# Optimization experiments

Measured on AMD Instinct MI355X. Metric: run time of the kernel, lower is better.

## Reference

```python
import jax, jax.numpy as jnp
import numpy as np

B, C, H, W = 8, 256, 64, 64
E, D, K = 4, 4, 2
CR = C // 16  # CBAM channel-attention reduction ratio 16

def _conv(x, w, pad):
    return jax.lax.conv_general_dilated(
        x, w, (1, 1), [(pad, pad), (pad, pad)],
        dimension_numbers=('NCHW', 'OIHW', 'NCHW'))

def _bn(x, s, b):  # eval-mode BatchNorm folded into per-channel affine
    return x * s[None, :, None, None] + b[None, :, None, None]

def _expert(p, x, dom_ids):
    # domain_transform: conv3x3-BN-GELU-conv3x3-BN
    h = jax.nn.gelu(_bn(_conv(x, p['dt_w1'], 1), p['dt_bn1s'], p['dt_bn1b']))
    d = _bn(_conv(h, p['dt_w2'], 1), p['dt_bn2s'], p['dt_bn2b'])
    # domain_gate: GAP -> conv1x1 C->1 -> sigmoid
    g1 = jax.nn.sigmoid(jnp.mean(d, (2, 3)) @ p['gate_w'] + p['gate_b'])  # [B]
    out = x + g1[:, None, None, None] * d
    # Res_CBAM_block (in==out channels, stride 1 -> identity shortcut)
    r = out
    h = jax.nn.relu(_bn(_conv(out, p['c1_w'], 1) + p['c1_b'][None, :, None, None], p['bn1s'], p['bn1b']))
    h = _bn(_conv(h, p['c2_w'], 1) + p['c2_b'][None, :, None, None], p['bn2s'], p['bn2b'])
    # channel attention (shared MLP over GAP and GMP)
    avg, mx = jnp.mean(h, (2, 3)), jnp.max(h, (2, 3))
    mlp = lambda v: jax.nn.relu(v @ p['ca_w1'].T) @ p['ca_w2'].T
    ca = jax.nn.sigmoid(mlp(avg) + mlp(mx))  # [B,C]
    h = h * ca[:, :, None, None]
    # spatial attention: 7x7 conv over [mean_c, max_c]
    sa_in = jnp.concatenate([jnp.mean(h, 1, keepdims=True), jnp.max(h, 1, keepdims=True)], axis=1)
    sa = jax.nn.sigmoid(_conv(sa_in, p['sa_w'], 3))
    h = jax.nn.relu(h * sa + r)
    # per-domain adapter bias (nn.Embedding lookup)
    return h + p['adp'][dom_ids][:, :, None, None]

def _forward(x, domain_ids, g_w1, g_b1, ln_s, ln_b, g_w2, g_b2, dom_emb,
             e_dt_w1, e_dt_bn1s, e_dt_bn1b, e_dt_w2, e_dt_bn2s, e_dt_bn2b,
             e_gate_w, e_gate_b, e_c1_w, e_c1_b, e_bn1s, e_bn1b,
             e_c2_w, e_c2_b, e_bn2s, e_bn2b, e_ca_w1, e_ca_w2, e_sa_w, e_adapter):
    ep = dict(dt_w1=e_dt_w1, dt_bn1s=e_dt_bn1s, dt_bn1b=e_dt_bn1b,
              dt_w2=e_dt_w2, dt_bn2s=e_dt_bn2s, dt_bn2b=e_dt_bn2b,
              gate_w=e_gate_w, gate_b=e_gate_b,
              c1_w=e_c1_w, c1_b=e_c1_b, bn1s=e_bn1s, bn1b=e_bn1b,
              c2_w=e_c2_w, c2_b=e_c2_b, bn2s=e_bn2s, bn2b=e_bn2b,
              ca_w1=e_ca_w1, ca_w2=e_ca_w2, sa_w=e_sa_w, adp=e_adapter)
    eouts = jax.vmap(_expert, in_axes=(0, None, None))(ep, x, domain_ids)  # [E,B,C,H,W]
    # gate input: [GAP(x) | GMP(x) | domain_embed(16)] -> Linear -> LN -> ReLU -> Linear -> softmax
    gi = jnp.concatenate([jnp.mean(x, (2, 3)), jnp.max(x, (2, 3)), dom_emb[domain_ids]], axis=1)
    hg = gi @ g_w1 + g_b1
    mu = jnp.mean(hg, -1, keepdims=True)
    var = jnp.var(hg, -1, keepdims=True)
    hg = jax.nn.relu((hg - mu) * jax.lax.rsqrt(var + 1e-5) * ln_s + ln_b)
    probs = jax.nn.softmax(hg @ g_w2 + g_b2, axis=-1)  # [B,E]
    vals, idx = jax.lax.top_k(probs, K)                # soft top-k routing
    wk = vals / jnp.sum(vals, -1, keepdims=True)       # renormalize top-k weights
    wfull = jnp.zeros_like(probs).at[jnp.arange(probs.shape[0])[:, None], idx].set(wk)
    return jnp.einsum('be,ebchw->bchw', wfull, eouts)

def setup_inputs():
    key = jax.random.key(0)
    ks = iter(jax.random.split(key, 48))
    rn = lambda shape, s=0.05: jax.random.normal(next(ks), shape, jnp.float32) * s
    p = {}
    p['x'] = jax.random.normal(next(ks), (B, C, H, W), jnp.float32)
    p['domain_ids'] = jax.random.randint(next(ks), (B,), 0, D)
    p['g_w1'] = rn((2 * C + 16, C)); p['g_b1'] = jnp.zeros((C,))
    p['ln_s'] = jnp.ones((C,)); p['ln_b'] = jnp.zeros((C,))
    p['g_w2'] = rn((C, E)); p['g_b2'] = jnp.zeros((E,))
    p['dom_emb'] = rn((D, 16), 0.5)
    p['e_dt_w1'] = rn((E, C, C, 3, 3)); p['e_dt_bn1s'] = jnp.ones((E, C)); p['e_dt_bn1b'] = jnp.zeros((E, C))
    p['e_dt_w2'] = rn((E, C, C, 3, 3)); p['e_dt_bn2s'] = jnp.ones((E, C)); p['e_dt_bn2b'] = jnp.zeros((E, C))
    p['e_gate_w'] = rn((E, C)); p['e_gate_b'] = jnp.zeros((E,))
    p['e_c1_w'] = rn((E, C, C, 3, 3)); p['e_c1_b'] = jnp.zeros((E, C))
    p['e_bn1s'] = jnp.ones((E, C)); p['e_bn1b'] = jnp.zeros((E, C))
    p['e_c2_w'] = rn((E, C, C, 3, 3)); p['e_c2_b'] = jnp.zeros((E, C))
    p['e_bn2s'] = jnp.ones((E, C)); p['e_bn2b'] = jnp.zeros((E, C))
    p['e_ca_w1'] = rn((E, CR, C)); p['e_ca_w2'] = rn((E, C, CR))
    p['e_sa_w'] = rn((E, 1, 2, 7, 7))
    p['e_adapter'] = rn((E, D, C), 0.1)
    return p

def reference(x, domain_ids, g_w1, g_b1, ln_s, ln_b, g_w2, g_b2, dom_emb,
              e_dt_w1, e_dt_bn1s, e_dt_bn1b, e_dt_w2, e_dt_bn2s, e_dt_bn2b,
              e_gate_w, e_gate_b, e_c1_w, e_c1_b, e_bn1s, e_bn1b,
              e_c2_w, e_c2_b, e_bn2s, e_bn2b, e_ca_w1, e_ca_w2, e_sa_w, e_adapter):
    return _forward(x, domain_ids, g_w1, g_b1, ln_s, ln_b, g_w2, g_b2, dom_emb,
                    e_dt_w1, e_dt_bn1s, e_dt_bn1b, e_dt_w2, e_dt_bn2s, e_dt_bn2b,
                    e_gate_w, e_gate_b, e_c1_w, e_c1_b, e_bn1s, e_bn1b,
                    e_c2_w, e_c2_b, e_bn2s, e_bn2b, e_ca_w1, e_ca_w2, e_sa_w, e_adapter)
```

## Files before the change

kernel.cpp:

```cpp
#include <hip/hip_runtime.h>
#include <math.h>

typedef __bf16 bf16x8 __attribute__((ext_vector_type(8)));
typedef float  f32x4  __attribute__((ext_vector_type(4)));

#define NB 8
#define NC 256
#define NHW 4096
#define NCHW_ 1048576
#define NSLOT 16

__device__ __forceinline__ float sigmoidf_(float x){ return 1.f/(1.f+expf(-x)); }
__device__ __forceinline__ float gelu_tanh(float x){
  float x3 = x*x*x;
  return 0.5f*x*(1.f+tanhf(0.7978845608028654f*(x + 0.044715f*x3)));
}

__device__ __forceinline__ void gload16(const void* g, void* l){
  __builtin_amdgcn_global_load_lds((const __attribute__((address_space(1))) void*)g,
                                   (__attribute__((address_space(3))) void*)l,
                                   16, 0, 0);
}

__global__ void k_prep_sb(const float* dt_bn1s, const float* dt_bn1b,
                          const float* dt_bn2s, const float* dt_bn2b,
                          const float* c1_b, const float* bn1s, const float* bn1b,
                          const float* c2_b, const float* bn2s, const float* bn2b,
                          float* effS, float* effB){
  int ec = blockIdx.x; int e = ec>>2, cv = ec&3; int c = threadIdx.x;
  int i = e*NC + c;
  float s, b;
  if (cv==0){ s = dt_bn1s[i]; b = dt_bn1b[i]; }
  else if (cv==1){ s = dt_bn2s[i]; b = dt_bn2b[i]; }
  else if (cv==2){ s = bn1s[i]; b = c1_b[i]*bn1s[i] + bn1b[i]; }
  else { s = bn2s[i]; b = c2_b[i]*bn2s[i] + bn2b[i]; }
  effS[ec*NC+c]=s; effB[ec*NC+c]=b;
}

__global__ void k_prep_w(const float* w0, const float* w1, const float* w2, const float* w3,
                         __bf16* wr){
  __shared__ float tl[9][257];
  int o = blockIdx.x; int ec = blockIdx.y; int e = ec>>2, cv = ec&3;
  int t = threadIdx.x;
  const float* src = (cv==0)?w0 : (cv==1)?w1 : (cv==2)?w2 : w3;
  const float* sp = src + ((size_t)((e*NC + o)*NC + t))*9;
  #pragma unroll
  for (int k=0;k<9;k++) tl[k][t] = sp[k];
  __syncthreads();
  __bf16* dst = wr + (size_t)ec*589824 + (size_t)o*256;
  #pragma unroll
  for (int k=0;k<9;k++) dst[(size_t)k*65536 + t] = (__bf16)tl[k][t];
}

__global__ void k_prep_x(const float* x, __bf16* xh){
  __shared__ float tl[32][33];
  int p0 = blockIdx.x*32, c0 = blockIdx.y*32, b = blockIdx.z;
  int tx = threadIdx.x&31, ty = threadIdx.x>>5;
  #pragma unroll
  for (int k=0;k<4;k++){
    int c = c0 + ty + k*8;
    tl[ty+k*8][tx] = x[(size_t)(b*NC+c)*NHW + p0 + tx];
  }
  __syncthreads();
  #pragma unroll
  for (int k=0;k<4;k++){
    int p = p0 + ty + k*8;
    xh[(size_t)b*NCHW_ + (size_t)p*NC + c0 + tx] = (__bf16)tl[tx][ty+k*8];
  }
}

__global__ void k_gate1(const float* x, float* gavg, float* gmax){
  __shared__ float rs[256], rm[256];
  int bc = blockIdx.x; int t = threadIdx.x;
  const float* base = x + (size_t)bc*NHW;
  float s=0.f, m=-1e30f;
  #pragma unroll
  for (int k=0;k<16;k++){ float v = base[t + k*256]; s+=v; m=fmaxf(m,v); }
  rs[t]=s; rm[t]=m; __syncthreads();
  for (int st=128; st; st>>=1){ if (t<st){ rs[t]+=rs[t+st]; rm[t]=fmaxf(rm[t],rm[t+st]); } __syncthreads(); }
  if (t==0){ gavg[bc]=rs[0]/4096.f; gmax[bc]=rm[0]; }
}

__global__ void k_gate2(const float* gavg, const float* gmax, const int* dom,
                        const float* dom_emb, const float* w1, const float* b1,
                        const float* lns, const float* lnb,
                        const float* w2, const float* b2,
                        int* slot_e, float* slot_w){
  __shared__ float gi[8][528];
  __shared__ float hg[8][256];
  __shared__ float stat[16];
  __shared__ float logit[8][4];
  int t = threadIdx.x;
  for (int idx=t; idx<8*528; idx+=256){
    int b = idx/528, k = idx - b*528;
    float v;
    if (k<256) v = gavg[b*256+k];
    else if (k<512) v = gmax[b*256+k-256];
    else v = dom_emb[dom[b]*16 + (k-512)];
    gi[b][k]=v;
  }
  __syncthreads();
  for (int b=0;b<8;b++){
    float acc = b1[t];
    for (int k=0;k<528;k++) acc += gi[b][k]*w1[k*256+t];
    hg[b][t]=acc;
  }
  __syncthreads();
  if (t<8){
    float mu=0.f; for(int c=0;c<256;c++) mu += hg[t][c]; mu/=256.f;
    float vr=0.f; for(int c=0;c<256;c++){ float d=hg[t][c]-mu; vr+=d*d; } vr/=256.f;
    stat[t]=mu; stat[8+t]=vr;
  }
  __syncthreads();
  for (int b=0;b<8;b++){
    float v = (hg[b][t]-stat[b])*rsqrtf(stat[8+b]+1e-5f)*lns[t]+lnb[t];
    hg[b][t] = fmaxf(v, 0.f);
  }
  __syncthreads();
  if (t<32){
    int b = t>>2, e = t&3;
    float acc = b2[e];
    for (int c=0;c<256;c++) acc += hg[b][c]*w2[c*4+e];
    logit[b][e]=acc;
  }
  __syncthreads();
  if (t==0){
    for (int b=0;b<8;b++){
      float mx = logit[b][0];
      for (int e=1;e<4;e++) mx = fmaxf(mx, logit[b][e]);
      float p[4], s=0.f;
      for (int e=0;e<4;e++){ p[e]=expf(logit[b][e]-mx); s+=p[e]; }
      for (int e=0;e<4;e++) p[e]/=s;
      int i0=0; for (int e=1;e<4;e++) if (p[e]>p[i0]) i0=e;
      int i1=-1; for (int e=0;e<4;e++){ if (e==i0) continue; if (i1<0 || p[e]>p[i1]) i1=e; }
      float den = p[i0]+p[i1];
      slot_e[2*b]   = i0; slot_w[2*b]   = p[i0]/den;
      slot_e[2*b+1] = i1; slot_w[2*b+1] = p[i1]/den;
    }
  }
}

template<int ACT>
__global__ __launch_bounds__(256,2) void k_conv(
    const __bf16* __restrict__ in0, int per_b,
    const __bf16* __restrict__ wr,  int conv_idx,
    const float* __restrict__ effS, const float* __restrict__ effB,
    const int* __restrict__ slot_e,
    const __bf16* __restrict__ zslab,
    __bf16* __restrict__ out)
{
  __shared__ __bf16 smem[17408];
  __bf16* lA = smem;
  __bf16* lB = smem + 8192;

  const int tid   = threadIdx.x;
  const int slot  = blockIdx.y;
  const int e     = slot_e[slot];
  const int tileM = blockIdx.x & 1;
  const int tileN = blockIdx.x >> 1;
  const int cout_base = tileM*128;
  const int pos_base  = tileN*128;
  const int lane   = tid & 63;
  const int wv     = tid >> 6;
  const int lane15 = lane & 15, quad = lane >> 4;
  const int m_off  = (wv&1)*64, n_off = (wv>>1)*64;

  const __bf16* in = in0 + (size_t)(per_b ? (slot>>1) : slot) * NCHW_;
  const __bf16* wb = wr + (size_t)(e*4 + conv_idx) * 589824;

  int ldsOff[4];
  int aOff[4];
  int bBase[4];
  int rr0[4], cl0[4];
  #pragma unroll
  for (int j=0;j<4;j++){
    int f = (wv*4+j)*64 + lane;
    int row = f>>3, ph = f&7;
    int lc = ph ^ (row&7);
    ldsOff[j] = f*8;
    aOff[j]   = (cout_base + row)*256 + lc*8;
    int gp = pos_base + row;
    rr0[j] = gp>>6; cl0[j] = gp&63;
    bBase[j] = lc*8;
  }

  f32x4 zero = {0.f,0.f,0.f,0.f};
  f32x4 acc[4][4];
  #pragma unroll
  for (int i=0;i<4;i++)
    #pragma unroll
    for (int j=0;j<4;j++) acc[i][j] = zero;

  const int ph_read = lane15 & 7;

  for (int kk=0; kk<36; ++kk){
    const int k9 = kk>>2, c0e = (kk&3)*64;
    const int k3 = k9/3;
    const int dy = k3 - 1, dx = k9 - k3*3 - 1;
    __syncthreads();
    {
      const __bf16* ws = wb + (size_t)k9*65536 + c0e;
      #pragma unroll
      for (int j=0;j<4;j++)
        gload16(ws + aOff[j], lA + ldsOff[j]);
    }
    {
      const int doff = dy*16384 + dx*256 + c0e;
      #pragma unroll
      for (int j=0;j<4;j++){
        int rr = rr0[j] + dy, cl = cl0[j] + dx;
        const __bf16* src = ((unsigned)rr < 64u && (unsigned)cl < 64u)
            ? in + (size_t)(rr0[j]*16384 + cl0[j]*256 + doff + bBase[j])
            : zslab;
        gload16(src, lB + ldsOff[j]);
      }
    }
    __syncthreads();
    #pragma unroll
    for (int s=0;s<2;s++){
      bf16x8 af[4], bfr[4];
      const int ph = (s*4 + quad) ^ ph_read;
      #pragma unroll
      for (int i=0;i<4;i++) af[i]  = *(const bf16x8*)(lA + (m_off + i*16 + lane15)*64 + ph*8);
      #pragma unroll
      for (int j=0;j<4;j++) bfr[j] = *(const bf16x8*)(lB + (n_off + j*16 + lane15)*64 + ph*8);
      #pragma unroll
      for (int i=0;i<4;i++)
        #pragma unroll
        for (int j=0;j<4;j++)
          acc[i][j] = __builtin_amdgcn_mfma_f32_16x16x32_bf16(af[i], bfr[j], acc[i][j], 0,0,0);
    }
  }
  __syncthreads();

  const float* sS = effS + (e*4+conv_idx)*256 + cout_base;
  const float* sB = effB + (e*4+conv_idx)*256 + cout_base;
  float sc[16], bi[16];
  #pragma unroll
  for (int i=0;i<4;i++)
    #pragma unroll
    for (int r=0;r<4;r++){
      int m = m_off + i*16 + quad*4 + r;
      sc[i*4+r] = sS[m]; bi[i*4+r] = sB[m];
    }
  __bf16* lO = smem;
  #pragma unroll
  for (int i=0;i<4;i++){
    #pragma unroll
    for (int j=0;j<4;j++){
      int n = n_off + j*16 + lane15;
      #pragma unroll
      for (int r=0;r<4;r++){
        int m = m_off + i*16 + quad*4 + r;
        float v = acc[i][j][r]*sc[i*4+r] + bi[i*4+r];
        if (ACT==1) v = gelu_tanh(v);
        if (ACT==2) v = fmaxf(v, 0.f);
        lO[n*136 + m] = (__bf16)v;
      }
    }
  }
  __syncthreads();
  __bf16* ob = out + (size_t)slot*NCHW_;
  #pragma unroll
  for (int h=0; h<8; ++h){
    int chunk = tid + h*256;
    int prow = chunk>>4, part = chunk&15;
    *(uint4*)(ob + (size_t)(pos_base+prow)*256 + cout_base + part*8) =
      *(const uint4*)(lO + prow*136 + part*8);
  }
}

__global__ void k_g1red(const __bf16* d, const float* gate_w, const int* slot_e, float* p_sum){
  __shared__ float red[256];
  int chunk = blockIdx.x, slot = blockIdx.y, t = threadIdx.x;
  int e = slot_e[slot];
  const __bf16* base = d + (size_t)slot*NCHW_ + (size_t)chunk*512*256;
  float s = 0.f;
  for (int p=0;p<512;p++) s += (float)base[(size_t)p*256 + t];
  s *= gate_w[e*256+t];
  red[t]=s; __syncthreads();
  for (int st=128; st; st>>=1){ if (t<st) red[t]+=red[t+st]; __syncthreads(); }
  if (t==0) p_sum[slot*8+chunk]=red[0];
}

__global__ void k_pw_r(const __bf16* xh, const __bf16* d, const float* p_sum,
                       const float* gate_b, const int* slot_e, __bf16* r){
  int slot = blockIdx.y;
  int idx = blockIdx.x*256 + threadIdx.x;
  float tot = 0.f;
  #pragma unroll
  for (int k=0;k<8;k++) tot += p_sum[slot*8+k];
  int e = slot_e[slot];
  float g1 = sigmoidf_(tot/4096.f + gate_b[e]);
  size_t o = (size_t)slot*NCHW_ + idx;
  r[o] = (__bf16)((float)xh[(size_t)(slot>>1)*NCHW_ + idx] + g1*(float)d[o]);
}

__global__ void k_ca1(const __bf16* h3, float* ps, float* pm){
  int chunk = blockIdx.x, slot = blockIdx.y, t = threadIdx.x;
  const __bf16* base = h3 + (size_t)slot*NCHW_ + (size_t)chunk*512*256;
  float s=0.f, m=-1e30f;
  for (int p=0;p<512;p++){ float v = (float)base[(size_t)p*256+t]; s+=v; m=fmaxf(m,v); }
  ps[(slot*8+chunk)*256+t]=s; pm[(slot*8+chunk)*256+t]=m;
}

__global__ void k_ca2(const float* ps, const float* pm, const float* w1, const float* w2,
                      const int* slot_e, float* ca){
  __shared__ float avg[256], mxs[256], hr[32];
  int slot = blockIdx.x, t = threadIdx.x;
  int e = slot_e[slot];
  float s=0.f, m=-1e30f;
  #pragma unroll
  for (int k=0;k<8;k++){ s += ps[(slot*8+k)*256+t]; m = fmaxf(m, pm[(slot*8+k)*256+t]); }
  avg[t]=s/4096.f; mxs[t]=m;
  __syncthreads();
  if (t<32){
    int j = t&15; int which = t>>4;
    const float* v = which? mxs : avg;
    float acc=0.f;
    for (int c=0;c<256;c++) acc += v[c]*w1[e*4096 + j*256 + c];
    hr[t] = fmaxf(acc, 0.f);
  }
  __syncthreads();
  float acc=0.f;
  #pragma unroll
  for (int j=0;j<16;j++) acc += (hr[j]+hr[16+j])*w2[e*4096 + t*16 + j];
  ca[slot*256+t] = sigmoidf_(acc);
}

__global__ void k_sa1(const __bf16* h3, const float* ca, float* sam){
  int slot = blockIdx.y;
  int wv = threadIdx.x>>6, lane = threadIdx.x&63;
  int p = blockIdx.x*4 + wv;
  const __bf16* base = h3 + (size_t)slot*NCHW_ + (size_t)p*256 + lane*4;
  const float* cb = ca + slot*256 + lane*4;
  float s=0.f, m=-1e30f;
  #pragma unroll
  for (int k=0;k<4;k++){ float v = (float)base[k]*cb[k]; s+=v; m=fmaxf(m,v); }
  #pragma unroll
  for (int off=32; off; off>>=1){ s += __shfl_down(s, off); m = fmaxf(m, __shfl_down(m, off)); }
  if (lane==0){ sam[slot*8192 + p] = s/256.f; sam[slot*8192 + 4096 + p] = m; }
}

__global__ void k_sa2(const float* sam, const float* sa_w, const int* slot_e, float* sa){
  int slot = blockIdx.y;
  int p = blockIdx.x*256 + threadIdx.x;
  int e = slot_e[slot];
  int y = p>>6, x = p&63;
  const float* m0 = sam + slot*8192;
  const float* m1 = m0 + 4096;
  const float* w = sa_w + e*98;
  float acc = 0.f;
  for (int ky=0;ky<7;ky++){
    int yy = y + ky - 3;
    if ((unsigned)yy >= 64u) continue;
    for (int kx=0;kx<7;kx++){
      int xx = x + kx - 3;
      if ((unsigned)xx >= 64u) continue;
      acc += w[ky*7+kx]*m0[yy*64+xx] + w[49+ky*7+kx]*m1[yy*64+xx];
    }
  }
  sa[slot*4096+p] = sigmoidf_(acc);
}

__global__ void k_fin1(const __bf16* h3, const __bf16* r, const float* ca, const float* sa,
                       const int* slot_e, const float* slot_w, const float* adapter,
                       const int* dom, float* fo){
  int p = blockIdx.x, b = blockIdx.y, c = threadIdx.x;
  float acc = 0.f;
  #pragma unroll
  for (int k=0;k<2;k++){
    int s = b*2+k;
    int e = slot_e[s];
    float w = slot_w[s];
    size_t o = (size_t)s*NCHW_ + (size_t)p*256 + c;
    float v = (float)h3[o]*ca[s*256+c]*sa[s*4096+p] + (float)r[o];
    v = fmaxf(v, 0.f) + adapter[(e*4+dom[b])*256 + c];
    acc += w*v;
  }
  fo[((size_t)b*4096+p)*256 + c] = acc;
}

__global__ void k_fin2(const float* fo, float* out){
  __shared__ float tl[32][33];
  int p0 = blockIdx.x*32, c0 = blockIdx.y*32, b = blockIdx.z;
  int tx = threadIdx.x&31, ty = threadIdx.x>>5;
  #pragma unroll
  for (int k=0;k<4;k++){
    int p = p0 + ty + k*8;
    tl[ty+k*8][tx] = fo[((size_t)b*4096+p)*256 + c0+tx];
  }
  __syncthreads();
  #pragma unroll
  for (int k=0;k<4;k++){
    int c = c0 + ty + k*8;
    out[((size_t)b*256+c)*4096 + p0+tx] = tl[tx][ty+k*8];
  }
}

extern "C" void kernel_launch(void* const* d_in, const int* in_sizes, int n_in,
                              void* d_out, int out_size, void* d_ws, size_t ws_size,
                              hipStream_t stream){
  const float* x      = (const float*)d_in[0];
  const int*   dom    = (const int*)d_in[1];
  const float* g_w1   = (const float*)d_in[2];
  const float* g_b1   = (const float*)d_in[3];
  const float* ln_s   = (const float*)d_in[4];
  const float* ln_b   = (const float*)d_in[5];
  const float* g_w2   = (const float*)d_in[6];
  const float* g_b2   = (const float*)d_in[7];
  const float* dom_emb= (const float*)d_in[8];
  const float* dt_w1  = (const float*)d_in[9];
  const float* dt_bn1s= (const float*)d_in[10];
  const float* dt_bn1b= (const float*)d_in[11];
  const float* dt_w2  = (const float*)d_in[12];
  const float* dt_bn2s= (const float*)d_in[13];
  const float* dt_bn2b= (const float*)d_in[14];
  const float* gate_w = (const float*)d_in[15];
  const float* gate_b = (const float*)d_in[16];
  const float* c1_w   = (const float*)d_in[17];
  const float* c1_b   = (const float*)d_in[18];
  const float* bn1s   = (const float*)d_in[19];
  const float* bn1b   = (const float*)d_in[20];
  const float* c2_w   = (const float*)d_in[21];
  const float* c2_b   = (const float*)d_in[22];
  const float* bn2s   = (const float*)d_in[23];
  const float* bn2b   = (const float*)d_in[24];
  const float* ca_w1  = (const float*)d_in[25];
  const float* ca_w2  = (const float*)d_in[26];
  const float* sa_w   = (const float*)d_in[27];
  const float* adapter= (const float*)d_in[28];

  char* ws = (char*)d_ws;
  size_t off = 0;
  auto alloc = [&](size_t bytes)->void*{
    void* p = ws + off; off += (bytes + 255) & ~size_t(255); return p;
  };
  __bf16* wr   = (__bf16*)alloc(16ull*589824*2);
  __bf16* xh   = (__bf16*)alloc(8ull*NCHW_*2);
  __bf16* bufA = (__bf16*)alloc(16ull*NCHW_*2);
  __bf16* bufB = (__bf16*)alloc(16ull*NCHW_*2);
  __bf16* bufC = (__bf16*)alloc(16ull*NCHW_*2);
  float* gavg  = (float*)alloc(2048*4);
  float* gmax  = (float*)alloc(2048*4);
  float* effS  = (float*)alloc(4096*4);
  float* effB  = (float*)alloc(4096*4);
  int*   slot_e= (int*)alloc(64);
  float* slot_w= (float*)alloc(64);
  float* p_sum = (float*)alloc(16*8*4);
  float* ca_ps = (float*)alloc(16*8*256*4);
  float* ca_pm = (float*)alloc(16*8*256*4);
  float* ca    = (float*)alloc(16*256*4);
  float* sam   = (float*)alloc(16*8192*4);
  float* sa    = (float*)alloc(16*4096*4);
  __bf16* zslab= (__bf16*)alloc(512);
  float* fo    = (float*)(void*)bufA;

  hipMemsetAsync(zslab, 0, 512, stream);

  k_prep_sb<<<dim3(16), dim3(256), 0, stream>>>(dt_bn1s, dt_bn1b, dt_bn2s, dt_bn2b,
                                                c1_b, bn1s, bn1b, c2_b, bn2s, bn2b, effS, effB);
  k_prep_w<<<dim3(256,16), dim3(256), 0, stream>>>(dt_w1, dt_w2, c1_w, c2_w, wr);
  k_prep_x<<<dim3(128,8,8), dim3(256), 0, stream>>>(x, xh);
  k_gate1<<<dim3(2048), dim3(256), 0, stream>>>(x, gavg, gmax);
  k_gate2<<<dim3(1), dim3(256), 0, stream>>>(gavg, gmax, dom, dom_emb, g_w1, g_b1,
                                             ln_s, ln_b, g_w2, g_b2, slot_e, slot_w);
  k_conv<1><<<dim3(64,16), dim3(256), 0, stream>>>(xh, 1, wr, 0, effS, effB, slot_e, zslab, bufA);
  k_conv<0><<<dim3(64,16), dim3(256), 0, stream>>>(bufA, 0, wr, 1, effS, effB, slot_e, zslab, bufB);
  k_g1red<<<dim3(8,16), dim3(256), 0, stream>>>(bufB, gate_w, slot_e, p_sum);
  k_pw_r<<<dim3(4096,16), dim3(256), 0, stream>>>(xh, bufB, p_sum, gate_b, slot_e, bufC);
  k_conv<2><<<dim3(64,16), dim3(256), 0, stream>>>(bufC, 0, wr, 2, effS, effB, slot_e, zslab, bufA);
  k_conv<0><<<dim3(64,16), dim3(256), 0, stream>>>(bufA, 0, wr, 3, effS, effB, slot_e, zslab, bufB);
  k_ca1<<<dim3(8,16), dim3(256), 0, stream>>>(bufB, ca_ps, ca_pm);
  k_ca2<<<dim3(16), dim3(256), 0, stream>>>(ca_ps, ca_pm, ca_w1, ca_w2, slot_e, ca);
  k_sa1<<<dim3(1024,16), dim3(256), 0, stream>>>(bufB, ca, sam);
  k_sa2<<<dim3(16,16), dim3(256), 0, stream>>>(sam, sa_w, slot_e, sa);
  k_fin1<<<dim3(4096,8), dim3(256), 0, stream>>>(bufB, bufC, ca, sa, slot_e, slot_w,
                                                 adapter, dom, fo);
  k_fin2<<<dim3(128,8,8), dim3(256), 0, stream>>>(fo, (float*)d_out);
}
```

Measured before the change: 739.1 us.

## Fuse reductions into conv epilogues, merge final kernels, remap blocks per XCD

The gate's global-average and max pooling moves into the x transpose kernel as per-tile partials. The domain-gate and channel-attention reductions move into the conv epilogues, reading the output tile already in shared memory, so bufB is not re-read. k_fin1 and k_fin2 merge into one kernel, removing the fp32 intermediate round trip. The k_gate2 matmul is reordered so each thread keeps 8 batch accumulators. Conv blocks are remapped so each slot's tiles land on one XCD, which should improve L2 reuse of its expert weights.

```diff
diff --git a/kernel.cpp b/kernel.cpp
--- a/kernel.cpp
+++ b/kernel.cpp
@@ -52,9 +52,10 @@
   for (int k=0;k<9;k++) dst[(size_t)k*65536 + t] = (__bf16)tl[k][t];
 }
 
-__global__ void k_prep_x(const float* x, __bf16* xh){
+__global__ void k_prep_x(const float* x, __bf16* xh, float* gps, float* gpm){
   __shared__ float tl[32][33];
-  int p0 = blockIdx.x*32, c0 = blockIdx.y*32, b = blockIdx.z;
+  __shared__ float rs[256], rm[256];
+  int ptile = blockIdx.x, p0 = ptile*32, c0 = blockIdx.y*32, b = blockIdx.z;
   int tx = threadIdx.x&31, ty = threadIdx.x>>5;
   #pragma unroll
   for (int k=0;k<4;k++){
@@ -67,18 +68,30 @@
     int p = p0 + ty + k*8;
     xh[(size_t)b*NCHW_ + (size_t)p*NC + c0 + tx] = (__bf16)tl[tx][ty+k*8];
   }
-}
-
-__global__ void k_gate1(const float* x, float* gavg, float* gmax){
-  __shared__ float rs[256], rm[256];
-  int bc = blockIdx.x; int t = threadIdx.x;
-  const float* base = x + (size_t)bc*NHW;
+  int c_local = threadIdx.x & 31, seg = threadIdx.x >> 5;
   float s=0.f, m=-1e30f;
   #pragma unroll
-  for (int k=0;k<16;k++){ float v = base[t + k*256]; s+=v; m=fmaxf(m,v); }
-  rs[t]=s; rm[t]=m; __syncthreads();
-  for (int st=128; st; st>>=1){ if (t<st){ rs[t]+=rs[t+st]; rm[t]=fmaxf(rm[t],rm[t+st]); } __syncthreads(); }
-  if (t==0){ gavg[bc]=rs[0]/4096.f; gmax[bc]=rm[0]; }
+  for (int j=0;j<4;j++){ float v = tl[c_local][seg*4+j]; s+=v; m=fmaxf(m,v); }
+  rs[seg*32+c_local]=s; rm[seg*32+c_local]=m;
+  __syncthreads();
+  if (threadIdx.x < 32){
+    float ss=0.f, mm=-1e30f;
+    #pragma unroll
+    for (int g=0; g<8; g++){ ss += rs[g*32+threadIdx.x]; mm = fmaxf(mm, rm[g*32+threadIdx.x]); }
+    gps[(size_t)(b*128+ptile)*256 + c0 + threadIdx.x] = ss;
+    gpm[(size_t)(b*128+ptile)*256 + c0 + threadIdx.x] = mm;
+  }
+}
+
+__global__ void k_gate1b(const float* gps, const float* gpm, float* gavg, float* gmax){
+  int b = blockIdx.x, c = threadIdx.x;
+  float s=0.f, m=-1e30f;
+  for (int k=0;k<128;k++){
+    s += gps[(size_t)(b*128+k)*256 + c];
+    m = fmaxf(m, gpm[(size_t)(b*128+k)*256 + c]);
+  }
+  gavg[b*256+c] = s/4096.f;
+  gmax[b*256+c] = m;
 }
 
 __global__ void k_gate2(const float* gavg, const float* gmax, const int* dom,
@@ -86,24 +99,32 @@
                         const float* lns, const float* lnb,
                         const float* w2, const float* b2,
                         int* slot_e, float* slot_w){
-  __shared__ float gi[8][528];
+  __shared__ float giT[528][8];
   __shared__ float hg[8][256];
   __shared__ float stat[16];
   __shared__ float logit[8][4];
   int t = threadIdx.x;
   for (int idx=t; idx<8*528; idx+=256){
-    int b = idx/528, k = idx - b*528;
+    int b = idx&7, k = idx>>3;
     float v;
     if (k<256) v = gavg[b*256+k];
     else if (k<512) v = gmax[b*256+k-256];
     else v = dom_emb[dom[b]*16 + (k-512)];
-    gi[b][k]=v;
-  }
-  __syncthreads();
-  for (int b=0;b<8;b++){
-    float acc = b1[t];
-    for (int k=0;k<528;k++) acc += gi[b][k]*w1[k*256+t];
-    hg[b][t]=acc;
+    giT[k][b]=v;
+  }
+  __syncthreads();
+  {
+    float acc[8];
+    float bb = b1[t];
+    #pragma unroll
+    for (int b=0;b<8;b++) acc[b]=bb;
+    for (int k=0;k<528;k++){
+      float wv = w1[k*256+t];
+      #pragma unroll
+      for (int b=0;b<8;b++) acc[b] += giT[k][b]*wv;
+    }
+    #pragma unroll
+    for (int b=0;b<8;b++) hg[b][t]=acc[b];
   }
   __syncthreads();
   if (t<8){
@@ -140,24 +161,30 @@
   }
 }
 
-template<int ACT>
+template<int ACT, int RED>
 __global__ __launch_bounds__(256,2) void k_conv(
     const __bf16* __restrict__ in0, int per_b,
     const __bf16* __restrict__ wr,  int conv_idx,
     const float* __restrict__ effS, const float* __restrict__ effB,
     const int* __restrict__ slot_e,
     const __bf16* __restrict__ zslab,
-    __bf16* __restrict__ out)
+    __bf16* __restrict__ out,
+    const float* __restrict__ gate_w, float* __restrict__ p_sum,
+    float* __restrict__ ca_ps, float* __restrict__ ca_pm)
 {
   __shared__ __bf16 smem[17408];
   __bf16* lA = smem;
   __bf16* lB = smem + 8192;
 
   const int tid   = threadIdx.x;
-  const int slot  = blockIdx.y;
+  const int lin   = blockIdx.y*64 + blockIdx.x;
+  const int xcd   = lin & 7;
+  const int q     = lin >> 3;
+  const int slot  = (xcd<<1) | (q>>6);
+  const int t64   = q & 63;
+  const int tileM = t64 & 1;
+  const int tileN = t64 >> 1;
   const int e     = slot_e[slot];
-  const int tileM = blockIdx.x & 1;
-  const int tileN = blockIdx.x >> 1;
   const int cout_base = tileM*128;
   const int pos_base  = tileN*128;
   const int lane   = tid & 63;
@@ -268,40 +295,56 @@
     *(uint4*)(ob + (size_t)(pos_base+prow)*256 + cout_base + part*8) =
       *(const uint4*)(lO + prow*136 + part*8);
   }
-}
-
-__global__ void k_g1red(const __bf16* d, const float* gate_w, const int* slot_e, float* p_sum){
-  __shared__ float red[256];
-  int chunk = blockIdx.x, slot = blockIdx.y, t = threadIdx.x;
-  int e = slot_e[slot];
-  const __bf16* base = d + (size_t)slot*NCHW_ + (size_t)chunk*512*256;
-  float s = 0.f;
-  for (int p=0;p<512;p++) s += (float)base[(size_t)p*256 + t];
-  s *= gate_w[e*256+t];
-  red[t]=s; __syncthreads();
-  for (int st=128; st; st>>=1){ if (t<st) red[t]+=red[t+st]; __syncthreads(); }
-  if (t==0) p_sum[slot*8+chunk]=red[0];
-}
-
-__global__ void k_pw_r(const __bf16* xh, const __bf16* d, const float* p_sum,
-                       const float* gate_b, const int* slot_e, __bf16* r){
+
+  if (RED==1){
+    int m = tid & 127, half = tid >> 7;
+    float s = 0.f;
+    const __bf16* col = lO + (half*64)*136 + m;
+    #pragma unroll 8
+    for (int n=0;n<64;n++) s += (float)col[n*136];
+    s *= gate_w[e*256 + cout_base + m];
+    #pragma unroll
+    for (int off=32; off; off>>=1) s += __shfl_down(s, off);
+    __syncthreads();
+    float* scr = (float*)smem;
+    if (lane==0) scr[wv] = s;
+    __syncthreads();
+    if (tid==0) p_sum[slot*64 + tileN*2 + tileM] = scr[0]+scr[1]+scr[2]+scr[3];
+  }
+  if (RED==2){
+    int m = tid & 127, half = tid >> 7;
+    float s=0.f, mx=-1e30f;
+    const __bf16* col = lO + (half*64)*136 + m;
+    #pragma unroll 8
+    for (int n=0;n<64;n++){ float v = (float)col[n*136]; s+=v; mx=fmaxf(mx,v); }
+    __syncthreads();
+    float* scr = (float*)smem;
+    scr[half*128+m] = s; scr[256 + half*128+m] = mx;
+    __syncthreads();
+    if (tid<128){
+      float ts = scr[tid] + scr[128+tid];
+      float tm = fmaxf(scr[256+tid], scr[384+tid]);
+      ca_ps[(size_t)(slot*32+tileN)*256 + cout_base + tid] = ts;
+      ca_pm[(size_t)(slot*32+tileN)*256 + cout_base + tid] = tm;
+    }
+  }
+}
+
+__global__ void k_g1fin(const float* p_sum, const float* gate_b, const int* slot_e, float* g1s){
+  int t = threadIdx.x;
+  if (t<16){
+    float s=0.f;
+    for (int k=0;k<64;k++) s += p_sum[t*64+k];
+    g1s[t] = sigmoidf_(s/4096.f + gate_b[slot_e[t]]);
+  }
+}
+
+__global__ void k_pw_r(const __bf16* xh, const __bf16* d, const float* g1s, __bf16* r){
   int slot = blockIdx.y;
   int idx = blockIdx.x*256 + threadIdx.x;
-  float tot = 0.f;
-  #pragma unroll
-  for (int k=0;k<8;k++) tot += p_sum[slot*8+k];
-  int e = slot_e[slot];
-  float g1 = sigmoidf_(tot/4096.f + gate_b[e]);
+  float g1 = g1s[slot];
   size_t o = (size_t)slot*NCHW_ + idx;
   r[o] = (__bf16)((float)xh[(size_t)(slot>>1)*NCHW_ + idx] + g1*(float)d[o]);
-}
-
-__global__ void k_ca1(const __bf16* h3, float* ps, float* pm){
-  int chunk = blockIdx.x, slot = blockIdx.y, t = threadIdx.x;
-  const __bf16* base = h3 + (size_t)slot*NCHW_ + (size_t)chunk*512*256;
-  float s=0.f, m=-1e30f;
-  for (int p=0;p<512;p++){ float v = (float)base[(size_t)p*256+t]; s+=v; m=fmaxf(m,v); }
-  ps[(slot*8+chunk)*256+t]=s; pm[(slot*8+chunk)*256+t]=m;
 }
 
 __global__ void k_ca2(const float* ps, const float* pm, const float* w1, const float* w2,
@@ -311,7 +354,10 @@
   int e = slot_e[slot];
   float s=0.f, m=-1e30f;
   #pragma unroll
-  for (int k=0;k<8;k++){ s += ps[(slot*8+k)*256+t]; m = fmaxf(m, pm[(slot*8+k)*256+t]); }
+  for (int k=0;k<32;k++){
+    s += ps[(size_t)(slot*32+k)*256+t];
+    m = fmaxf(m, pm[(size_t)(slot*32+k)*256+t]);
+  }
   avg[t]=s/4096.f; mxs[t]=m;
   __syncthreads();
   if (t<32){
@@ -363,38 +409,33 @@
   sa[slot*4096+p] = sigmoidf_(acc);
 }
 
-__global__ void k_fin1(const __bf16* h3, const __bf16* r, const float* ca, const float* sa,
-                       const int* slot_e, const float* slot_w, const float* adapter,
-                       const int* dom, float* fo){
-  int p = blockIdx.x, b = blockIdx.y, c = threadIdx.x;
-  float acc = 0.f;
-  #pragma unroll
-  for (int k=0;k<2;k++){
-    int s = b*2+k;
-    int e = slot_e[s];
-    float w = slot_w[s];
-    size_t o = (size_t)s*NCHW_ + (size_t)p*256 + c;
-    float v = (float)h3[o]*ca[s*256+c]*sa[s*4096+p] + (float)r[o];
-    v = fmaxf(v, 0.f) + adapter[(e*4+dom[b])*256 + c];
-    acc += w*v;
-  }
-  fo[((size_t)b*4096+p)*256 + c] = acc;
-}
-
-__global__ void k_fin2(const float* fo, float* out){
+__global__ void k_fin(const __bf16* h3, const __bf16* r, const float* ca, const float* sa,
+                      const int* slot_e, const float* slot_w, const float* adapter,
+                      const int* dom, float* out){
   __shared__ float tl[32][33];
   int p0 = blockIdx.x*32, c0 = blockIdx.y*32, b = blockIdx.z;
   int tx = threadIdx.x&31, ty = threadIdx.x>>5;
+  int s0 = b*2, s1 = b*2+1;
+  int e0 = slot_e[s0], e1 = slot_e[s1];
+  float w0 = slot_w[s0], w1 = slot_w[s1];
+  int dm = dom[b];
+  int c = c0 + tx;
+  float ad = w0*adapter[(e0*4+dm)*256 + c] + w1*adapter[(e1*4+dm)*256 + c];
+  float ca0 = ca[s0*256+c], ca1 = ca[s1*256+c];
   #pragma unroll
   for (int k=0;k<4;k++){
     int p = p0 + ty + k*8;
-    tl[ty+k*8][tx] = fo[((size_t)b*4096+p)*256 + c0+tx];
+    size_t o0 = (size_t)s0*NCHW_ + (size_t)p*256 + c;
+    size_t o1 = (size_t)s1*NCHW_ + (size_t)p*256 + c;
+    float v0 = (float)h3[o0]*ca0*sa[s0*4096+p] + (float)r[o0];
+    float v1 = (float)h3[o1]*ca1*sa[s1*4096+p] + (float)r[o1];
+    tl[tx][ty+k*8] = w0*fmaxf(v0,0.f) + w1*fmaxf(v1,0.f) + ad;
   }
   __syncthreads();
   #pragma unroll
   for (int k=0;k<4;k++){
-    int c = c0 + ty + k*8;
-    out[((size_t)b*256+c)*4096 + p0+tx] = tl[tx][ty+k*8];
+    int cc = c0 + ty + k*8;
+    out[((size_t)(b*NC+cc))*NHW + p0 + tx] = tl[ty+k*8][tx];
   }
 }
 
@@ -441,41 +482,45 @@
   __bf16* bufA = (__bf16*)alloc(16ull*NCHW_*2);
   __bf16* bufB = (__bf16*)alloc(16ull*NCHW_*2);
   __bf16* bufC = (__bf16*)alloc(16ull*NCHW_*2);
+  float* gps   = (float*)alloc(8ull*128*256*4);
+  float* gpm   = (float*)alloc(8ull*128*256*4);
   float* gavg  = (float*)alloc(2048*4);
   float* gmax  = (float*)alloc(2048*4);
   float* effS  = (float*)alloc(4096*4);
   float* effB  = (float*)alloc(4096*4);
   int*   slot_e= (int*)alloc(64);
   float* slot_w= (float*)alloc(64);
-  float* p_sum = (float*)alloc(16*8*4);
-  float* ca_ps = (float*)alloc(16*8*256*4);
-  float* ca_pm = (float*)alloc(16*8*256*4);
+  float* p_sum = (float*)alloc(16*64*4);
+  float* g1s   = (float*)alloc(64);
+  float* ca_ps = (float*)alloc(16*32*256*4);
+  float* ca_pm = (float*)alloc(16*32*256*4);
   float* ca    = (float*)alloc(16*256*4);
   float* sam   = (float*)alloc(16*8192*4);
   float* sa    = (float*)alloc(16*4096*4);
   __bf16* zslab= (__bf16*)alloc(512);
-  float* fo    = (float*)(void*)bufA;
 
   hipMemsetAsync(zslab, 0, 512, stream);
 
   k_prep_sb<<<dim3(16), dim3(256), 0, stream>>>(dt_bn1s, dt_bn1b, dt_bn2s, dt_bn2b,
                                                 c1_b, bn1s, bn1b, c2_b, bn2s, bn2b, effS, effB);
   k_prep_w<<<dim3(256,16), dim3(256), 0, stream>>>(dt_w1, dt_w2, c1_w, c2_w, wr);
-  k_prep_x<<<dim3(128,8,8), dim3(256), 0, stream>>>(x, xh);
-  k_gate1<<<dim3(2048), dim3(256), 0, stream>>>(x, gavg, gmax);
+  k_prep_x<<<dim3(128,8,8), dim3(256), 0, stream>>>(x, xh, gps, gpm);
+  k_gate1b<<<dim3(8), dim3(256), 0, stream>>>(gps, gpm, gavg, gmax);
   k_gate2<<<dim3(1), dim3(256), 0, stream>>>(gavg, gmax, dom, dom_emb, g_w1, g_b1,
                                              ln_s, ln_b, g_w2, g_b2, slot_e, slot_w);
-  k_conv<1><<<dim3(64,16), dim3(256), 0, stream>>>(xh, 1, wr, 0, effS, effB, slot_e, zslab, bufA);
-  k_conv<0><<<dim3(64,16), dim3(256), 0, stream>>>(bufA, 0, wr, 1, effS, effB, slot_e, zslab, bufB);
-  k_g1red<<<dim3(8,16), dim3(256), 0, stream>>>(bufB, gate_w, slot_e, p_sum);
-  k_pw_r<<<dim3(4096,16), dim3(256), 0, stream>>>(xh, bufB, p_sum, gate_b, slot_e, bufC);
-  k_conv<2><<<dim3(64,16), dim3(256), 0, stream>>>(bufC, 0, wr, 2, effS, effB, slot_e, zslab, bufA);
-  k_conv<0><<<dim3(64,16), dim3(256), 0, stream>>>(bufA, 0, wr, 3, effS, effB, slot_e, zslab, bufB);
-  k_ca1<<<dim3(8,16), dim3(256), 0, stream>>>(bufB, ca_ps, ca_pm);
+  k_conv<1,0><<<dim3(64,16), dim3(256), 0, stream>>>(xh, 1, wr, 0, effS, effB, slot_e, zslab, bufA,
+                                                     gate_w, p_sum, ca_ps, ca_pm);
+  k_conv<0,1><<<dim3(64,16), dim3(256), 0, stream>>>(bufA, 0, wr, 1, effS, effB, slot_e, zslab, bufB,
+                                                     gate_w, p_sum, ca_ps, ca_pm);
+  k_g1fin<<<dim3(1), dim3(64), 0, stream>>>(p_sum, gate_b, slot_e, g1s);
+  k_pw_r<<<dim3(4096,16), dim3(256), 0, stream>>>(xh, bufB, g1s, bufC);
+  k_conv<2,0><<<dim3(64,16), dim3(256), 0, stream>>>(bufC, 0, wr, 2, effS, effB, slot_e, zslab, bufA,
+                                                     gate_w, p_sum, ca_ps, ca_pm);
+  k_conv<0,2><<<dim3(64,16), dim3(256), 0, stream>>>(bufA, 0, wr, 3, effS, effB, slot_e, zslab, bufB,
+                                                     gate_w, p_sum, ca_ps, ca_pm);
   k_ca2<<<dim3(16), dim3(256), 0, stream>>>(ca_ps, ca_pm, ca_w1, ca_w2, slot_e, ca);
   k_sa1<<<dim3(1024,16), dim3(256), 0, stream>>>(bufB, ca, sam);
   k_sa2<<<dim3(16,16), dim3(256), 0, stream>>>(sam, sa_w, slot_e, sa);
-  k_fin1<<<dim3(4096,8), dim3(256), 0, stream>>>(bufB, bufC, ca, sa, slot_e, slot_w,
-                                                 adapter, dom, fo);
-  k_fin2<<<dim3(128,8,8), dim3(256), 0, stream>>>(fo, (float*)d_out);
-}
+  k_fin<<<dim3(128,8,8), dim3(256), 0, stream>>>(bufB, bufC, ca, sa, slot_e, slot_w,
+                                                 adapter, dom, (float*)d_out);
+}
```

Result: faster. 615.6 us (-16.7%).
